# Kernel optimization log

Hardware: AMD Instinct MI355X
Metric: run time of the kernel (lower is better)

Reference implementation:

```python
import jax, jax.numpy as jnp
import numpy as np

SEP = 2            # sep_token_id
B, S, H = 8, 4096, 768
MAX_SENT = 64      # = labels.size(1) in the original
STD = 0.02         # initializer_range


def setup_inputs() -> dict:
    key = jax.random.key(0)
    ks = jax.random.split(key, 6)
    hidden = jax.random.normal(ks[0], (B, S, H), jnp.float32)
    ids = jax.random.randint(ks[1], (B, S), 5, 30000, dtype=jnp.int64)
    # plant a sep every 64 tokens -> 64 seps, 64 non-empty sentences per row
    ids = ids.at[:, 63::64].set(SEP)
    W1 = jax.random.normal(ks[2], (H, 4096), jnp.float32) * STD
    b1 = jnp.zeros((4096,), jnp.float32)
    W2 = jax.random.normal(ks[3], (4096, 256), jnp.float32) * STD
    b2 = jnp.zeros((256,), jnp.float32)
    W3 = jax.random.normal(ks[4], (256, 2), jnp.float32) * STD
    b3 = jnp.zeros((2,), jnp.float32)
    return dict(hidden=hidden, input_ids=ids, W1=W1, b1=b1, W2=W2, b2=b2, W3=W3, b3=b3)


def _pool_row(h, ids):
    # h: [S, H], ids: [S] -> per-sentence means [MAX_SENT, H]
    sep = (ids == SEP)
    sep_i = sep.astype(jnp.int32)
    # exclusive cumsum: segment id = number of seps strictly before position t
    seg = jnp.cumsum(sep_i) - sep_i
    pos = jnp.arange(S)
    first_sep = jnp.argmax(sep)
    n_sep = sep_i.sum()
    # original includes the FIRST sep in sentence 0 but excludes later seps,
    # and excludes the last token of the trailing (post-last-sep) segment
    weight = jnp.where(sep, pos == first_sep, True)
    weight = weight & ~((pos == S - 1) & (seg == n_sep) & (n_sep > 0))
    # truncate to max_sentences: overflow segments land in a dump bucket
    seg_c = jnp.minimum(seg, MAX_SENT)
    hw = jnp.where(weight[:, None], h, 0.0)
    sums = jax.ops.segment_sum(hw, seg_c, num_segments=MAX_SENT + 1)[:MAX_SENT]
    cnts = jax.ops.segment_sum(weight.astype(h.dtype), seg_c, num_segments=MAX_SENT + 1)[:MAX_SENT]
    # empty (padding) segments -> zeros, matching the original zero-padding
    return jnp.where(cnts[:, None] > 0, sums / jnp.maximum(cnts, 1.0)[:, None], 0.0)


def reference(hidden, input_ids, W1, b1, W2, b2, W3, b3):
    # [B, MAX_SENT, H] per-sentence mean representations
    sent = jax.vmap(_pool_row)(hidden, input_ids)
    # classifier head (dropout = identity in eval); GELU is exact (torch nn.GELU default)
    x = jax.nn.gelu(jnp.einsum('bmh,hf->bmf', sent, W1) + b1, approximate=False)
    x = jax.nn.gelu(jnp.einsum('bmf,fg->bmg', x, W2) + b2, approximate=False)
    logits = jnp.einsum('bmg,gc->bmc', x, W3) + b3  # [B, MAX_SENT, 2]
    return logits
```

## Files before the change

kernel.cpp:

```cpp
#include <hip/hip_runtime.h>
#include <hip/hip_bf16.h>

#define SEP_ID 2
#define S_LEN  4096
#define HID    768
#define MAXS   64

using short8  = __attribute__((ext_vector_type(8))) short;
using floatx4 = __attribute__((ext_vector_type(4))) float;

__global__ void bounds_kernel(const int* __restrict__ ids,
                              int* __restrict__ sent_start,
                              int* __restrict__ sent_cnt) {
    const int b = blockIdx.x;
    const int t = threadIdx.x;
    const int* row = ids + (size_t)b * S_LEN;

    __shared__ int cnts[256];
    __shared__ int offs[256];
    __shared__ int sep_pos[S_LEN];
    __shared__ int total;

    int local[16];
    int c = 0;
    const int base = t * 16;
    #pragma unroll
    for (int i = 0; i < 16; ++i) {
        if (row[base + i] == SEP_ID) local[c++] = base + i;
    }
    cnts[t] = c;
    __syncthreads();
    if (t == 0) {
        int s = 0;
        for (int i = 0; i < 256; ++i) { offs[i] = s; s += cnts[i]; }
        total = s;
    }
    __syncthreads();
    {
        int o = offs[t];
        for (int i = 0; i < c; ++i) sep_pos[o + i] = local[i];
    }
    __syncthreads();

    const int n_sep = total;
    if (t < MAXS) {
        const int m = t;
        int start = 0, cnt = 0;
        if (n_sep == 0) {
            if (m == 0) { start = 0; cnt = S_LEN; }
        } else if (m < n_sep) {
            if (m == 0) { start = 0; cnt = sep_pos[0] + 1; }
            else { start = sep_pos[m - 1] + 1; cnt = sep_pos[m] - sep_pos[m - 1] - 1; }
        } else if (m == n_sep) {
            start = sep_pos[n_sep - 1] + 1;
            cnt = (S_LEN - 1) - start;
            if (cnt < 0) cnt = 0;
        }
        sent_start[b * MAXS + m] = start;
        sent_cnt[b * MAXS + m]  = cnt;
    }
}

__global__ __launch_bounds__(192) void pool_kernel(const float* __restrict__ hidden,
                                                   const int* __restrict__ sent_start,
                                                   const int* __restrict__ sent_cnt,
                                                   __hip_bfloat16* __restrict__ sent) {
    const int blk = blockIdx.x;
    const int b = blk >> 6;
    const int t = threadIdx.x;
    const int start = sent_start[blk];
    const int cnt   = sent_cnt[blk];

    const float4* base = (const float4*)(hidden + ((size_t)b * S_LEN + start) * HID);
    float ax = 0.f, ay = 0.f, az = 0.f, aw = 0.f;
    int i = 0;
    for (; i + 4 <= cnt; i += 4) {
        float4 v0 = base[(size_t)(i + 0) * 192 + t];
        float4 v1 = base[(size_t)(i + 1) * 192 + t];
        float4 v2 = base[(size_t)(i + 2) * 192 + t];
        float4 v3 = base[(size_t)(i + 3) * 192 + t];
        ax += v0.x + v1.x + v2.x + v3.x;
        ay += v0.y + v1.y + v2.y + v3.y;
        az += v0.z + v1.z + v2.z + v3.z;
        aw += v0.w + v1.w + v2.w + v3.w;
    }
    for (; i < cnt; ++i) {
        float4 v = base[(size_t)i * 192 + t];
        ax += v.x; ay += v.y; az += v.z; aw += v.w;
    }
    const float inv = (cnt > 0) ? 1.0f / (float)cnt : 0.0f;
    __hip_bfloat16* o = sent + (size_t)blk * HID + t * 4;
    o[0] = __float2bfloat16(ax * inv);
    o[1] = __float2bfloat16(ay * inv);
    o[2] = __float2bfloat16(az * inv);
    o[3] = __float2bfloat16(aw * inv);
}

__global__ __launch_bounds__(256) void tconv_kernel(const float* __restrict__ W1,
                                                    const float* __restrict__ W2,
                                                    __hip_bfloat16* __restrict__ W1T,
                                                    __hip_bfloat16* __restrict__ W2T) {
    __shared__ float tile[32][33];
    int id = blockIdx.x;
    const float* in; __hip_bfloat16* out; int K, N, n0, k0;
    if (id < 3072) {
        in = W1; out = W1T; K = 768; N = 4096;
        n0 = (id & 127) * 32; k0 = (id >> 7) * 32;
    } else {
        id -= 3072;
        in = W2; out = W2T; K = 4096; N = 256;
        n0 = (id & 7) * 32; k0 = (id >> 3) * 32;
    }
    const int c = threadIdx.x & 31;
    const int r = threadIdx.x >> 5;
    #pragma unroll
    for (int i = 0; i < 32; i += 8)
        tile[r + i][c] = in[(size_t)(k0 + r + i) * N + n0 + c];
    __syncthreads();
    #pragma unroll
    for (int i = 0; i < 32; i += 8)
        out[(size_t)(n0 + r + i) * K + k0 + c] = __float2bfloat16(tile[c][r + i]);
}

__device__ __forceinline__ float gelu_exact(float x) {
    return 0.5f * x * (1.0f + erff(x * 0.70710678118654752f));
}

__global__ __launch_bounds__(256) void gemm1_kernel(const __hip_bfloat16* __restrict__ A,
                                                    const __hip_bfloat16* __restrict__ BT,
                                                    const float* __restrict__ bias,
                                                    __hip_bfloat16* __restrict__ out) {
    const int n0 = blockIdx.x * 128;
    const int m0 = blockIdx.y * 64;
    const int t = threadIdx.x;
    const int w = t >> 6, l = t & 63;
    const int wm = (w >> 1) * 32;
    const int wn = (w & 1) * 64;

    __shared__ __hip_bfloat16 Al[64][40];
    __shared__ __hip_bfloat16 Bl[128][40];

    floatx4 acc[2][4] = {};

    const int r  = t >> 2;
    const int ch = (t & 3) * 8;
    const __hip_bfloat16* Ag  = A  + (size_t)(m0 + r) * 768 + ch;
    const __hip_bfloat16* Bg0 = BT + (size_t)(n0 + r) * 768 + ch;
    const __hip_bfloat16* Bg1 = BT + (size_t)(n0 + 64 + r) * 768 + ch;

    const int lr = l & 15;
    const int kq = (l >> 4) * 8;

    for (int k0 = 0; k0 < 768; k0 += 32) {
        short8 av  = *(const short8*)(Ag  + k0);
        short8 bv0 = *(const short8*)(Bg0 + k0);
        short8 bv1 = *(const short8*)(Bg1 + k0);
        __syncthreads();
        *(short8*)(&Al[r][ch])      = av;
        *(short8*)(&Bl[r][ch])      = bv0;
        *(short8*)(&Bl[64 + r][ch]) = bv1;
        __syncthreads();

        short8 a0 = *(const short8*)(&Al[wm + lr][kq]);
        short8 a1 = *(const short8*)(&Al[wm + 16 + lr][kq]);
        #pragma unroll
        for (int j = 0; j < 4; ++j) {
            short8 bj = *(const short8*)(&Bl[wn + j * 16 + lr][kq]);
            acc[0][j] = __builtin_amdgcn_mfma_f32_16x16x32_bf16(a0, bj, acc[0][j], 0, 0, 0);
            acc[1][j] = __builtin_amdgcn_mfma_f32_16x16x32_bf16(a1, bj, acc[1][j], 0, 0, 0);
        }
    }

    #pragma unroll
    for (int i = 0; i < 2; ++i) {
        #pragma unroll
        for (int j = 0; j < 4; ++j) {
            const int col  = n0 + wn + j * 16 + lr;
            const int rowb = m0 + wm + i * 16 + (l >> 4) * 4;
            const float bv = bias[col];
            #pragma unroll
            for (int rg = 0; rg < 4; ++rg) {
                float x = acc[i][j][rg] + bv;
                out[(size_t)(rowb + rg) * 4096 + col] = __float2bfloat16(gelu_exact(x));
            }
        }
    }
}

__global__ __launch_bounds__(256) void gemm2_kernel(const __hip_bfloat16* __restrict__ A,
                                                    const __hip_bfloat16* __restrict__ BT,
                                                    float* __restrict__ part) {
    const int n0 = blockIdx.x * 64;
    const int m0 = blockIdx.y * 64;
    const int s  = blockIdx.z;
    const int kb = s * 512;
    const int t = threadIdx.x;
    const int w = t >> 6, l = t & 63;
    const int wm = (w >> 1) * 32;
    const int wn = (w & 1) * 32;

    __shared__ __hip_bfloat16 Al[64][40];
    __shared__ __hip_bfloat16 Bl[64][40];

    floatx4 acc[2][2] = {};

    const int r  = t >> 2;
    const int ch = (t & 3) * 8;
    const __hip_bfloat16* Ag = A  + (size_t)(m0 + r) * 4096 + kb + ch;
    const __hip_bfloat16* Bg = BT + (size_t)(n0 + r) * 4096 + kb + ch;

    const int lr = l & 15;
    const int kq = (l >> 4) * 8;

    for (int k0 = 0; k0 < 512; k0 += 32) {
        short8 av = *(const short8*)(Ag + k0);
        short8 bv = *(const short8*)(Bg + k0);
        __syncthreads();
        *(short8*)(&Al[r][ch]) = av;
        *(short8*)(&Bl[r][ch]) = bv;
        __syncthreads();

        short8 a0 = *(const short8*)(&Al[wm + lr][kq]);
        short8 a1 = *(const short8*)(&Al[wm + 16 + lr][kq]);
        short8 b0 = *(const short8*)(&Bl[wn + lr][kq]);
        short8 b1 = *(const short8*)(&Bl[wn + 16 + lr][kq]);

        acc[0][0] = __builtin_amdgcn_mfma_f32_16x16x32_bf16(a0, b0, acc[0][0], 0, 0, 0);
        acc[0][1] = __builtin_amdgcn_mfma_f32_16x16x32_bf16(a0, b1, acc[0][1], 0, 0, 0);
        acc[1][0] = __builtin_amdgcn_mfma_f32_16x16x32_bf16(a1, b0, acc[1][0], 0, 0, 0);
        acc[1][1] = __builtin_amdgcn_mfma_f32_16x16x32_bf16(a1, b1, acc[1][1], 0, 0, 0);
    }

    float* po = part + (size_t)s * 512 * 256;
    #pragma unroll
    for (int i = 0; i < 2; ++i) {
        #pragma unroll
        for (int j = 0; j < 2; ++j) {
            const int col  = n0 + wn + j * 16 + lr;
            const int rowb = m0 + wm + i * 16 + (l >> 4) * 4;
            #pragma unroll
            for (int rg = 0; rg < 4; ++rg)
                po[(size_t)(rowb + rg) * 256 + col] = acc[i][j][rg];
        }
    }
}

__global__ __launch_bounds__(256) void rh_kernel(const float* __restrict__ part,
                                                 const float* __restrict__ b2,
                                                 const float* __restrict__ W3,
                                                 const float* __restrict__ b3,
                                                 float* __restrict__ out) {
    const int row = blockIdx.x;
    const int c = threadIdx.x;
    const int w = c >> 6, l = c & 63;

    float s = 0.f;
    #pragma unroll
    for (int k = 0; k < 8; ++k)
        s += part[((size_t)k * 512 + row) * 256 + c];
    const float x = gelu_exact(s + b2[c]);
    float y0 = x * W3[c * 2 + 0];
    float y1 = x * W3[c * 2 + 1];
    #pragma unroll
    for (int off = 32; off; off >>= 1) {
        y0 += __shfl_down(y0, off);
        y1 += __shfl_down(y1, off);
    }
    __shared__ float r0[4], r1[4];
    if (l == 0) { r0[w] = y0; r1[w] = y1; }
    __syncthreads();
    if (c == 0) out[row * 2 + 0] = r0[0] + r0[1] + r0[2] + r0[3] + b3[0];
    if (c == 1) out[row * 2 + 1] = r1[0] + r1[1] + r1[2] + r1[3] + b3[1];
}

extern "C" void kernel_launch(void* const* d_in, const int* in_sizes, int n_in,
                              void* d_out, int out_size, void* d_ws, size_t ws_size,
                              hipStream_t stream) {
    const float* hidden = (const float*)d_in[0];
    const int*   ids    = (const int*)d_in[1];
    const float* W1     = (const float*)d_in[2];
    const float* b1     = (const float*)d_in[3];
    const float* W2     = (const float*)d_in[4];
    const float* b2     = (const float*)d_in[5];
    const float* W3     = (const float*)d_in[6];
    const float* b3     = (const float*)d_in[7];
    float* out = (float*)d_out;

    char* ws = (char*)d_ws;
    int* sent_start        = (int*)(ws + 0);
    int* sent_cnt          = (int*)(ws + 2048);
    __hip_bfloat16* sentb  = (__hip_bfloat16*)(ws + 4096);
    __hip_bfloat16* W1T    = (__hip_bfloat16*)(ws + 790528);
    __hip_bfloat16* W2T    = (__hip_bfloat16*)(ws + 7081984);
    __hip_bfloat16* x1     = (__hip_bfloat16*)(ws + 9179136);
    float* part            = (float*)(ws + 13373440);

    bounds_kernel<<<8, 256, 0, stream>>>(ids, sent_start, sent_cnt);
    pool_kernel<<<512, 192, 0, stream>>>(hidden, sent_start, sent_cnt, sentb);
    tconv_kernel<<<4096, 256, 0, stream>>>(W1, W2, W1T, W2T);
    gemm1_kernel<<<dim3(32, 8), 256, 0, stream>>>(sentb, W1T, b1, x1);
    gemm2_kernel<<<dim3(4, 8, 8), 256, 0, stream>>>(x1, W2T, part);
    rh_kernel<<<512, 256, 0, stream>>>(part, b2, W3, b3, out);
}
```

Measured before the change: 207.8 us.

## Fuse bounds and weight-transpose kernels, retile GEMMs with deeper K steps and more splits

Merges the sentence-bounds scan and the weight transpose/convert into a single launch, and replaces the serial prefix sum with a wave-shuffle scan. The pooling loop unrolls to 8 outstanding loads. gemm1 moves to 64x64 tiles (twice as many blocks), and both GEMMs stage 64-wide K tiles so each barrier pair covers two MFMA steps. gemm2 uses 16 K-splits instead of 8, which doubles the partial-sum traffic that the reduction kernel has to read.

```diff
diff --git a/kernel.cpp b/kernel.cpp
--- a/kernel.cpp
+++ b/kernel.cpp
@@ -9,55 +9,87 @@
 using short8  = __attribute__((ext_vector_type(8))) short;
 using floatx4 = __attribute__((ext_vector_type(4))) float;
 
-__global__ void bounds_kernel(const int* __restrict__ ids,
-                              int* __restrict__ sent_start,
-                              int* __restrict__ sent_cnt) {
-    const int b = blockIdx.x;
+__device__ __forceinline__ float gelu_exact(float x) {
+    return 0.5f * x * (1.0f + erff(x * 0.70710678118654752f));
+}
+
+__global__ __launch_bounds__(256) void prep_kernel(const int* __restrict__ ids,
+                                                   const float* __restrict__ W1,
+                                                   const float* __restrict__ W2,
+                                                   __hip_bfloat16* __restrict__ W1T,
+                                                   __hip_bfloat16* __restrict__ W2T,
+                                                   int* __restrict__ sent_start,
+                                                   int* __restrict__ sent_cnt) {
+    __shared__ __align__(16) char smem[16896];
+    const int blk = blockIdx.x;
     const int t = threadIdx.x;
-    const int* row = ids + (size_t)b * S_LEN;
-
-    __shared__ int cnts[256];
-    __shared__ int offs[256];
-    __shared__ int sep_pos[S_LEN];
-    __shared__ int total;
-
-    int local[16];
-    int c = 0;
-    const int base = t * 16;
-    #pragma unroll
-    for (int i = 0; i < 16; ++i) {
-        if (row[base + i] == SEP_ID) local[c++] = base + i;
-    }
-    cnts[t] = c;
-    __syncthreads();
-    if (t == 0) {
-        int s = 0;
-        for (int i = 0; i < 256; ++i) { offs[i] = s; s += cnts[i]; }
-        total = s;
-    }
-    __syncthreads();
-    {
-        int o = offs[t];
+
+    if (blk < 8) {
+        int* sep_pos = (int*)smem;
+        int* wtot    = sep_pos + 4096;
+        const int b = blk;
+        const int* row = ids + (size_t)b * S_LEN;
+        const int lane = t & 63, w = t >> 6;
+
+        int local[16]; int c = 0;
+        const int base = t * 16;
+        #pragma unroll
+        for (int q = 0; q < 4; ++q) {
+            int4 v = ((const int4*)row)[t * 4 + q];
+            if (v.x == SEP_ID) local[c++] = base + q * 4 + 0;
+            if (v.y == SEP_ID) local[c++] = base + q * 4 + 1;
+            if (v.z == SEP_ID) local[c++] = base + q * 4 + 2;
+            if (v.w == SEP_ID) local[c++] = base + q * 4 + 3;
+        }
+        int scan = c;
+        #pragma unroll
+        for (int off = 1; off < 64; off <<= 1) {
+            int n = __shfl_up(scan, off);
+            if (lane >= off) scan += n;
+        }
+        if (lane == 63) wtot[w] = scan;
+        __syncthreads();
+        int wbase = 0;
+        for (int i = 0; i < w; ++i) wbase += wtot[i];
+        const int o = wbase + scan - c;
         for (int i = 0; i < c; ++i) sep_pos[o + i] = local[i];
-    }
-    __syncthreads();
-
-    const int n_sep = total;
-    if (t < MAXS) {
-        const int m = t;
-        int start = 0, cnt = 0;
-        if (n_sep == 0) {
-            if (m == 0) { start = 0; cnt = S_LEN; }
-        } else if (m < n_sep) {
-            if (m == 0) { start = 0; cnt = sep_pos[0] + 1; }
-            else { start = sep_pos[m - 1] + 1; cnt = sep_pos[m] - sep_pos[m - 1] - 1; }
-        } else if (m == n_sep) {
-            start = sep_pos[n_sep - 1] + 1;
-            cnt = (S_LEN - 1) - start;
-            if (cnt < 0) cnt = 0;
-        }
-        sent_start[b * MAXS + m] = start;
-        sent_cnt[b * MAXS + m]  = cnt;
+        __syncthreads();
+        const int n_sep = wtot[0] + wtot[1] + wtot[2] + wtot[3];
+
+        if (t < MAXS) {
+            const int m = t;
+            int start = 0, cnt = 0;
+            if (n_sep == 0) {
+                if (m == 0) { start = 0; cnt = S_LEN; }
+            } else if (m < n_sep) {
+                if (m == 0) { start = 0; cnt = sep_pos[0] + 1; }
+                else { start = sep_pos[m - 1] + 1; cnt = sep_pos[m] - sep_pos[m - 1] - 1; }
+            } else if (m == n_sep) {
+                start = sep_pos[n_sep - 1] + 1;
+                cnt = (S_LEN - 1) - start;
+                if (cnt < 0) cnt = 0;
+            }
+            sent_start[b * MAXS + m] = start;
+            sent_cnt[b * MAXS + m]  = cnt;
+        }
+    } else {
+        float* tile = (float*)smem;
+        const int id0 = blk - 8;
+        const float* in; __hip_bfloat16* outw; int K, N, n0, k0;
+        if (id0 < 3072) { in = W1; outw = W1T; K = 768;  N = 4096;
+                          n0 = (id0 & 127) * 32; k0 = (id0 >> 7) * 32; }
+        else { const int id = id0 - 3072;
+               in = W2; outw = W2T; K = 4096; N = 256;
+               n0 = (id & 7) * 32; k0 = (id >> 3) * 32; }
+        const int c = t & 31;
+        const int r = t >> 5;
+        #pragma unroll
+        for (int i = 0; i < 32; i += 8)
+            tile[(r + i) * 33 + c] = in[(size_t)(k0 + r + i) * N + n0 + c];
+        __syncthreads();
+        #pragma unroll
+        for (int i = 0; i < 32; i += 8)
+            outw[(size_t)(n0 + r + i) * K + k0 + c] = __float2bfloat16(tile[c * 33 + r + i]);
     }
 }
 
@@ -74,15 +106,12 @@
     const float4* base = (const float4*)(hidden + ((size_t)b * S_LEN + start) * HID);
     float ax = 0.f, ay = 0.f, az = 0.f, aw = 0.f;
     int i = 0;
-    for (; i + 4 <= cnt; i += 4) {
-        float4 v0 = base[(size_t)(i + 0) * 192 + t];
-        float4 v1 = base[(size_t)(i + 1) * 192 + t];
-        float4 v2 = base[(size_t)(i + 2) * 192 + t];
-        float4 v3 = base[(size_t)(i + 3) * 192 + t];
-        ax += v0.x + v1.x + v2.x + v3.x;
-        ay += v0.y + v1.y + v2.y + v3.y;
-        az += v0.z + v1.z + v2.z + v3.z;
-        aw += v0.w + v1.w + v2.w + v3.w;
+    for (; i + 8 <= cnt; i += 8) {
+        float4 v[8];
+        #pragma unroll
+        for (int j = 0; j < 8; ++j) v[j] = base[(size_t)(i + j) * 192 + t];
+        #pragma unroll
+        for (int j = 0; j < 8; ++j) { ax += v[j].x; ay += v[j].y; az += v[j].z; aw += v[j].w; }
     }
     for (; i < cnt; ++i) {
         float4 v = base[(size_t)i * 192 + t];
@@ -96,85 +125,59 @@
     o[3] = __float2bfloat16(aw * inv);
 }
 
-__global__ __launch_bounds__(256) void tconv_kernel(const float* __restrict__ W1,
-                                                    const float* __restrict__ W2,
-                                                    __hip_bfloat16* __restrict__ W1T,
-                                                    __hip_bfloat16* __restrict__ W2T) {
-    __shared__ float tile[32][33];
-    int id = blockIdx.x;
-    const float* in; __hip_bfloat16* out; int K, N, n0, k0;
-    if (id < 3072) {
-        in = W1; out = W1T; K = 768; N = 4096;
-        n0 = (id & 127) * 32; k0 = (id >> 7) * 32;
-    } else {
-        id -= 3072;
-        in = W2; out = W2T; K = 4096; N = 256;
-        n0 = (id & 7) * 32; k0 = (id >> 3) * 32;
-    }
-    const int c = threadIdx.x & 31;
-    const int r = threadIdx.x >> 5;
-    #pragma unroll
-    for (int i = 0; i < 32; i += 8)
-        tile[r + i][c] = in[(size_t)(k0 + r + i) * N + n0 + c];
-    __syncthreads();
-    #pragma unroll
-    for (int i = 0; i < 32; i += 8)
-        out[(size_t)(n0 + r + i) * K + k0 + c] = __float2bfloat16(tile[c][r + i]);
-}
-
-__device__ __forceinline__ float gelu_exact(float x) {
-    return 0.5f * x * (1.0f + erff(x * 0.70710678118654752f));
-}
-
 __global__ __launch_bounds__(256) void gemm1_kernel(const __hip_bfloat16* __restrict__ A,
                                                     const __hip_bfloat16* __restrict__ BT,
                                                     const float* __restrict__ bias,
                                                     __hip_bfloat16* __restrict__ out) {
-    const int n0 = blockIdx.x * 128;
+    const int n0 = blockIdx.x * 64;
     const int m0 = blockIdx.y * 64;
     const int t = threadIdx.x;
     const int w = t >> 6, l = t & 63;
     const int wm = (w >> 1) * 32;
-    const int wn = (w & 1) * 64;
-
-    __shared__ __hip_bfloat16 Al[64][40];
-    __shared__ __hip_bfloat16 Bl[128][40];
-
-    floatx4 acc[2][4] = {};
+    const int wn = (w & 1) * 32;
+
+    __shared__ __hip_bfloat16 Al[64][72];
+    __shared__ __hip_bfloat16 Bl[64][72];
+
+    floatx4 acc[2][2] = {};
 
     const int r  = t >> 2;
-    const int ch = (t & 3) * 8;
-    const __hip_bfloat16* Ag  = A  + (size_t)(m0 + r) * 768 + ch;
-    const __hip_bfloat16* Bg0 = BT + (size_t)(n0 + r) * 768 + ch;
-    const __hip_bfloat16* Bg1 = BT + (size_t)(n0 + 64 + r) * 768 + ch;
+    const int ch = (t & 3) * 16;
+    const __hip_bfloat16* Ag = A  + (size_t)(m0 + r) * 768 + ch;
+    const __hip_bfloat16* Bg = BT + (size_t)(n0 + r) * 768 + ch;
 
     const int lr = l & 15;
     const int kq = (l >> 4) * 8;
 
-    for (int k0 = 0; k0 < 768; k0 += 32) {
-        short8 av  = *(const short8*)(Ag  + k0);
-        short8 bv0 = *(const short8*)(Bg0 + k0);
-        short8 bv1 = *(const short8*)(Bg1 + k0);
-        __syncthreads();
-        *(short8*)(&Al[r][ch])      = av;
-        *(short8*)(&Bl[r][ch])      = bv0;
-        *(short8*)(&Bl[64 + r][ch]) = bv1;
-        __syncthreads();
-
-        short8 a0 = *(const short8*)(&Al[wm + lr][kq]);
-        short8 a1 = *(const short8*)(&Al[wm + 16 + lr][kq]);
-        #pragma unroll
-        for (int j = 0; j < 4; ++j) {
-            short8 bj = *(const short8*)(&Bl[wn + j * 16 + lr][kq]);
-            acc[0][j] = __builtin_amdgcn_mfma_f32_16x16x32_bf16(a0, bj, acc[0][j], 0, 0, 0);
-            acc[1][j] = __builtin_amdgcn_mfma_f32_16x16x32_bf16(a1, bj, acc[1][j], 0, 0, 0);
+    for (int k0 = 0; k0 < 768; k0 += 64) {
+        short8 av0 = *(const short8*)(Ag + k0);
+        short8 av1 = *(const short8*)(Ag + k0 + 8);
+        short8 bv0 = *(const short8*)(Bg + k0);
+        short8 bv1 = *(const short8*)(Bg + k0 + 8);
+        __syncthreads();
+        *(short8*)(&Al[r][ch])     = av0;
+        *(short8*)(&Al[r][ch + 8]) = av1;
+        *(short8*)(&Bl[r][ch])     = bv0;
+        *(short8*)(&Bl[r][ch + 8]) = bv1;
+        __syncthreads();
+
+        #pragma unroll
+        for (int ks = 0; ks < 64; ks += 32) {
+            short8 a0 = *(const short8*)(&Al[wm + lr][ks + kq]);
+            short8 a1 = *(const short8*)(&Al[wm + 16 + lr][ks + kq]);
+            short8 b0 = *(const short8*)(&Bl[wn + lr][ks + kq]);
+            short8 b1 = *(const short8*)(&Bl[wn + 16 + lr][ks + kq]);
+            acc[0][0] = __builtin_amdgcn_mfma_f32_16x16x32_bf16(a0, b0, acc[0][0], 0, 0, 0);
+            acc[0][1] = __builtin_amdgcn_mfma_f32_16x16x32_bf16(a0, b1, acc[0][1], 0, 0, 0);
+            acc[1][0] = __builtin_amdgcn_mfma_f32_16x16x32_bf16(a1, b0, acc[1][0], 0, 0, 0);
+            acc[1][1] = __builtin_amdgcn_mfma_f32_16x16x32_bf16(a1, b1, acc[1][1], 0, 0, 0);
         }
     }
 
     #pragma unroll
     for (int i = 0; i < 2; ++i) {
         #pragma unroll
-        for (int j = 0; j < 4; ++j) {
+        for (int j = 0; j < 2; ++j) {
             const int col  = n0 + wn + j * 16 + lr;
             const int rowb = m0 + wm + i * 16 + (l >> 4) * 4;
             const float bv = bias[col];
@@ -193,42 +196,48 @@
     const int n0 = blockIdx.x * 64;
     const int m0 = blockIdx.y * 64;
     const int s  = blockIdx.z;
-    const int kb = s * 512;
+    const int kb = s * 256;
     const int t = threadIdx.x;
     const int w = t >> 6, l = t & 63;
     const int wm = (w >> 1) * 32;
     const int wn = (w & 1) * 32;
 
-    __shared__ __hip_bfloat16 Al[64][40];
-    __shared__ __hip_bfloat16 Bl[64][40];
+    __shared__ __hip_bfloat16 Al[64][72];
+    __shared__ __hip_bfloat16 Bl[64][72];
 
     floatx4 acc[2][2] = {};
 
     const int r  = t >> 2;
-    const int ch = (t & 3) * 8;
+    const int ch = (t & 3) * 16;
     const __hip_bfloat16* Ag = A  + (size_t)(m0 + r) * 4096 + kb + ch;
     const __hip_bfloat16* Bg = BT + (size_t)(n0 + r) * 4096 + kb + ch;
 
     const int lr = l & 15;
     const int kq = (l >> 4) * 8;
 
-    for (int k0 = 0; k0 < 512; k0 += 32) {
-        short8 av = *(const short8*)(Ag + k0);
-        short8 bv = *(const short8*)(Bg + k0);
-        __syncthreads();
-        *(short8*)(&Al[r][ch]) = av;
-        *(short8*)(&Bl[r][ch]) = bv;
-        __syncthreads();
-
-        short8 a0 = *(const short8*)(&Al[wm + lr][kq]);
-        short8 a1 = *(const short8*)(&Al[wm + 16 + lr][kq]);
-        short8 b0 = *(const short8*)(&Bl[wn + lr][kq]);
-        short8 b1 = *(const short8*)(&Bl[wn + 16 + lr][kq]);
-
-        acc[0][0] = __builtin_amdgcn_mfma_f32_16x16x32_bf16(a0, b0, acc[0][0], 0, 0, 0);
-        acc[0][1] = __builtin_amdgcn_mfma_f32_16x16x32_bf16(a0, b1, acc[0][1], 0, 0, 0);
-        acc[1][0] = __builtin_amdgcn_mfma_f32_16x16x32_bf16(a1, b0, acc[1][0], 0, 0, 0);
-        acc[1][1] = __builtin_amdgcn_mfma_f32_16x16x32_bf16(a1, b1, acc[1][1], 0, 0, 0);
+    for (int k0 = 0; k0 < 256; k0 += 64) {
+        short8 av0 = *(const short8*)(Ag + k0);
+        short8 av1 = *(const short8*)(Ag + k0 + 8);
+        short8 bv0 = *(const short8*)(Bg + k0);
+        short8 bv1 = *(const short8*)(Bg + k0 + 8);
+        __syncthreads();
+        *(short8*)(&Al[r][ch])     = av0;
+        *(short8*)(&Al[r][ch + 8]) = av1;
+        *(short8*)(&Bl[r][ch])     = bv0;
+        *(short8*)(&Bl[r][ch + 8]) = bv1;
+        __syncthreads();
+
+        #pragma unroll
+        for (int ks = 0; ks < 64; ks += 32) {
+            short8 a0 = *(const short8*)(&Al[wm + lr][ks + kq]);
+            short8 a1 = *(const short8*)(&Al[wm + 16 + lr][ks + kq]);
+            short8 b0 = *(const short8*)(&Bl[wn + lr][ks + kq]);
+            short8 b1 = *(const short8*)(&Bl[wn + 16 + lr][ks + kq]);
+            acc[0][0] = __builtin_amdgcn_mfma_f32_16x16x32_bf16(a0, b0, acc[0][0], 0, 0, 0);
+            acc[0][1] = __builtin_amdgcn_mfma_f32_16x16x32_bf16(a0, b1, acc[0][1], 0, 0, 0);
+            acc[1][0] = __builtin_amdgcn_mfma_f32_16x16x32_bf16(a1, b0, acc[1][0], 0, 0, 0);
+            acc[1][1] = __builtin_amdgcn_mfma_f32_16x16x32_bf16(a1, b1, acc[1][1], 0, 0, 0);
+        }
     }
 
     float* po = part + (size_t)s * 512 * 256;
@@ -256,7 +265,7 @@
 
     float s = 0.f;
     #pragma unroll
-    for (int k = 0; k < 8; ++k)
+    for (int k = 0; k < 16; ++k)
         s += part[((size_t)k * 512 + row) * 256 + c];
     const float x = gelu_exact(s + b2[c]);
     float y0 = x * W3[c * 2 + 0];
@@ -295,10 +304,9 @@
     __hip_bfloat16* x1     = (__hip_bfloat16*)(ws + 9179136);
     float* part            = (float*)(ws + 13373440);
 
-    bounds_kernel<<<8, 256, 0, stream>>>(ids, sent_start, sent_cnt);
+    prep_kernel<<<4104, 256, 0, stream>>>(ids, W1, W2, W1T, W2T, sent_start, sent_cnt);
     pool_kernel<<<512, 192, 0, stream>>>(hidden, sent_start, sent_cnt, sentb);
-    tconv_kernel<<<4096, 256, 0, stream>>>(W1, W2, W1T, W2T);
-    gemm1_kernel<<<dim3(32, 8), 256, 0, stream>>>(sentb, W1T, b1, x1);
-    gemm2_kernel<<<dim3(4, 8, 8), 256, 0, stream>>>(x1, W2T, part);
+    gemm1_kernel<<<dim3(64, 8), 256, 0, stream>>>(sentb, W1T, b1, x1);
+    gemm2_kernel<<<dim3(4, 8, 16), 256, 0, stream>>>(x1, W2T, part);
     rh_kernel<<<512, 256, 0, stream>>>(part, b2, W3, b3, out);
 }
```

Result: faster. 199.0 us (-4.2%).
